# Kernel optimization log

Measured on AMD Instinct MI355X. Metric: run time of the kernel, lower is better.

## Reference

```python
import jax, jax.numpy as jnp
import numpy as np

D_MODEL = 1024


def setup_inputs() -> dict:
    key = jax.random.key(0)
    ks = jax.random.split(key, 7)
    x = jax.random.normal(ks[0], (4, 2048, D_MODEL), dtype=jnp.float32)
    scale = 1.0 / np.sqrt(D_MODEL)
    Wq = jax.random.normal(ks[1], (D_MODEL, D_MODEL), dtype=jnp.float32) * scale
    bq = jnp.zeros((D_MODEL,), dtype=jnp.float32)
    Wk = jax.random.normal(ks[2], (D_MODEL, D_MODEL), dtype=jnp.float32) * scale
    bk = jnp.zeros((D_MODEL,), dtype=jnp.float32)
    Wv = jax.random.normal(ks[3], (D_MODEL, D_MODEL), dtype=jnp.float32) * scale
    bv = jnp.zeros((D_MODEL,), dtype=jnp.float32)
    return {"x": x, "Wq": Wq, "bq": bq, "Wk": Wk, "bk": bk, "Wv": Wv, "bv": bv}


def reference(x, Wq, bq, Wk, bk, Wv, bv):
    # Linear layers: y = x @ W^T + b (torch nn.Linear convention)
    q = jnp.einsum("bsd,ed->bse", x, Wq) + bq
    k = jnp.einsum("bsd,ed->bse", x, Wk) + bk
    v = jnp.einsum("bsd,ed->bse", x, Wv) + bv
    d_k = q.shape[-1]
    inv_sqrt_dk = 1.0 / jnp.sqrt(jnp.float32(d_k))
    # [B, S, S] score matrix, softmax over keys, then AV
    score = jnp.einsum("bqd,bkd->bqk", q, k) * inv_sqrt_dk
    attn = jax.nn.softmax(score, axis=-1)
    out = jnp.einsum("bqk,bkd->bqd", attn, v)
    return out
```

## Files before the change

### kernel.cpp

```cpp
#include <hip/hip_runtime.h>
#include <hip/hip_bf16.h>


typedef __hip_bfloat16 bf16;
typedef __attribute__((ext_vector_type(8))) short bf16x8;
typedef __attribute__((ext_vector_type(4))) float f32x4;
typedef __attribute__((ext_vector_type(4))) short short4v;

__device__ __forceinline__ void gload16(const void* g, void* l) {
  __builtin_amdgcn_global_load_lds(
      (const __attribute__((address_space(1))) void*)g,
      (__attribute__((address_space(3))) void*)l, 16, 0, 0);
}

__global__ __launch_bounds__(256)
void cast_f32_to_bf16(const float* __restrict__ in, bf16* __restrict__ out) {
  long i = ((long)blockIdx.x * blockDim.x + threadIdx.x) * 4;
  float4 f = *(const float4*)(in + i);
  bf16 tmp[4];
  tmp[0] = __float2bfloat16(f.x);
  tmp[1] = __float2bfloat16(f.y);
  tmp[2] = __float2bfloat16(f.z);
  tmp[3] = __float2bfloat16(f.w);
  *(short4v*)(out + i) = *(short4v*)tmp;
}

template<int OMODE>
__global__ __launch_bounds__(256, 3)
void gemm_bt(const bf16* __restrict__ A, const bf16* __restrict__ Bt,
             const float* __restrict__ b0, const float* __restrict__ b1,
             const float* __restrict__ b2, void* __restrict__ Cout,
             int K, int lda, int ldb, int ldc, float scale,
             long sA, long sB, long sC)
{
  __shared__ __align__(16) bf16 As[128 * 64];
  __shared__ __align__(16) bf16 Bs[128 * 64];
  const int tid = threadIdx.x;
  const int z = blockIdx.z;
  const bf16* Ab = A + (long)z * sA;
  const bf16* Bb = Bt + (long)z * sB;
  const long bm = (long)blockIdx.x * 128;
  const long bn = (long)blockIdx.y * 128;
  const int wid = tid >> 6;
  const int lane = tid & 63;
  const int wr = (wid >> 1) * 64;
  const int wc = (wid & 1) * 64;
  const int l15 = lane & 15;
  const int kg = lane >> 4;

  f32x4 acc[4][4];
#pragma unroll
  for (int m = 0; m < 4; ++m)
#pragma unroll
    for (int n = 0; n < 4; ++n)
      acc[m][n] = (f32x4){0.f, 0.f, 0.f, 0.f};

  for (int k0 = 0; k0 < K; k0 += 64) {
#pragma unroll
    for (int i = 0; i < 4; ++i) {
      const int c = (i << 8) + tid;
      const int r = c >> 3;
      const int j = (c & 7) ^ (r & 7);
      const int ldsch = (i << 8) + (wid << 6);
      gload16(Ab + (long)(bm + r) * lda + k0 + (j << 3), (bf16*)As + ldsch * 8);
      gload16(Bb + (long)(bn + r) * ldb + k0 + (j << 3), (bf16*)Bs + ldsch * 8);
    }
    __syncthreads();
#pragma unroll
    for (int kk = 0; kk < 2; ++kk) {
      const int jp = ((kk << 2) + kg) ^ (l15 & 7);
      bf16x8 af[4], bfv[4];
#pragma unroll
      for (int m = 0; m < 4; ++m)
        af[m] = *(const bf16x8*)&As[(wr + (m << 4) + l15) * 64 + (jp << 3)];
#pragma unroll
      for (int n = 0; n < 4; ++n)
        bfv[n] = *(const bf16x8*)&Bs[(wc + (n << 4) + l15) * 64 + (jp << 3)];
#pragma unroll
      for (int m = 0; m < 4; ++m)
#pragma unroll
        for (int n = 0; n < 4; ++n)
          acc[m][n] = __builtin_amdgcn_mfma_f32_16x16x32_bf16(
              af[m], bfv[n], acc[m][n], 0, 0, 0);
    }
    __syncthreads();
  }

#pragma unroll
  for (int m = 0; m < 4; ++m) {
    const long row0 = bm + wr + (m << 4) + kg * 4;
#pragma unroll
    for (int n = 0; n < 4; ++n) {
      const long col = bn + wc + (n << 4) + l15;
      if constexpr (OMODE == 0) {
        float* C = (float*)Cout + z * sC;
#pragma unroll
        for (int r = 0; r < 4; ++r)
          C[(row0 + r) * ldc + col] = acc[m][n][r] * scale;
      } else {
        const float* bias = (z == 0) ? b0 : (z == 1) ? b1 : b2;
        const float bias_v = bias[col];
        if (z < 2) {
          bf16* C = (bf16*)Cout + (long)z * 8192 * 1024;
#pragma unroll
          for (int r = 0; r < 4; ++r)
            C[(row0 + r) * 1024 + col] = __float2bfloat16(acc[m][n][r] + bias_v);
        } else {
          bf16* C = (bf16*)Cout + 2L * 8192 * 1024;
          const long bb = row0 >> 11;
          const long s0 = row0 & 2047;
          bf16 tmp[4];
#pragma unroll
          for (int r = 0; r < 4; ++r)
            tmp[r] = __float2bfloat16(acc[m][n][r] + bias_v);
          *(short4v*)&C[(bb * 1024 + col) * 2048 + s0] = *(short4v*)tmp;
        }
      }
    }
  }
}

__global__ __launch_bounds__(256)
void softmax_inplace_bf16(float* __restrict__ S) {
  float* row = S + (size_t)blockIdx.x * 2048;
  const int tid = threadIdx.x;
  __shared__ float redA[4], redB[4];
  float v[8];
  float mx = -1e30f;
#pragma unroll
  for (int i = 0; i < 8; ++i) {
    v[i] = row[tid + (i << 8)];
    mx = fmaxf(mx, v[i]);
  }
#pragma unroll
  for (int o = 32; o; o >>= 1) mx = fmaxf(mx, __shfl_xor(mx, o));
  if ((tid & 63) == 0) redA[tid >> 6] = mx;
  __syncthreads();
  mx = fmaxf(fmaxf(redA[0], redA[1]), fmaxf(redA[2], redA[3]));
  float sum = 0.f;
#pragma unroll
  for (int i = 0; i < 8; ++i) {
    v[i] = __expf(v[i] - mx);
    sum += v[i];
  }
#pragma unroll
  for (int o = 32; o; o >>= 1) sum += __shfl_xor(sum, o);
  if ((tid & 63) == 0) redB[tid >> 6] = sum;
  __syncthreads();
  sum = redB[0] + redB[1] + redB[2] + redB[3];
  const float inv = 1.f / sum;
  bf16* po = (bf16*)row;
#pragma unroll
  for (int i = 0; i < 8; ++i)
    po[tid + (i << 8)] = __float2bfloat16(v[i] * inv);
}

extern "C" void kernel_launch(void* const* d_in, const int* in_sizes, int n_in,
                              void* d_out, int out_size, void* d_ws, size_t ws_size,
                              hipStream_t stream) {
  const float* x  = (const float*)d_in[0];
  const float* Wq = (const float*)d_in[1];
  const float* bq = (const float*)d_in[2];
  const float* Wk = (const float*)d_in[3];
  const float* bk = (const float*)d_in[4];
  const float* Wv = (const float*)d_in[5];
  const float* bv = (const float*)d_in[6];
  float* out = (float*)d_out;

  const int B = 4, S = 2048, D = 1024;
  const int M = B * S;

  bf16* xb  = (bf16*)d_ws;
  bf16* wqb = xb + (size_t)M * D;
  bf16* qb  = wqb + 3 * (size_t)D * D;
  bf16* kb  = qb + (size_t)M * D;
  bf16* vtb = kb + (size_t)M * D;
  float* sc = (float*)(vtb + (size_t)M * D);

  size_t avail = ws_size - ((size_t)((char*)sc - (char*)d_ws));
  int nb = (int)(avail / ((size_t)S * S * 4));
  if (nb > B) nb = B;
  if (nb < 1) nb = 1;

  cast_f32_to_bf16<<<dim3(M * D / 1024), 256, 0, stream>>>(x, xb);
  cast_f32_to_bf16<<<dim3(D * D / 1024), 256, 0, stream>>>(Wq, wqb);
  cast_f32_to_bf16<<<dim3(D * D / 1024), 256, 0, stream>>>(Wk, wqb + (size_t)D * D);
  cast_f32_to_bf16<<<dim3(D * D / 1024), 256, 0, stream>>>(Wv, wqb + 2 * (size_t)D * D);

  gemm_bt<3><<<dim3(M / 128, D / 128, 3), 256, 0, stream>>>(
      xb, wqb, bq, bk, bv, qb, D, D, D, D, 1.f, 0, (long)D * D, 0);

  const float iscale = 1.0f / 32.0f;
  for (int g = 0; g < B; g += nb) {
    const int gn = (g + nb <= B) ? nb : (B - g);
    gemm_bt<0><<<dim3(S / 128, S / 128, gn), 256, 0, stream>>>(
        qb + (size_t)g * S * D, kb + (size_t)g * S * D, nullptr, nullptr, nullptr,
        sc, D, D, D, S, iscale, (long)S * D, (long)S * D, (long)S * S);
    softmax_inplace_bf16<<<dim3(gn * S), 256, 0, stream>>>(sc);
    gemm_bt<0><<<dim3(S / 128, D / 128, gn), 256, 0, stream>>>(
        (const bf16*)sc, vtb + (size_t)g * D * S, nullptr, nullptr, nullptr,
        out + (size_t)g * S * D, S, 2 * S, S, D, 1.f,
        2L * S * S, (long)D * S, (long)S * D);
  }
}
```

Measured before the change: 178.7 us.

## Replace GEMMs with 8-wave double-buffered pipelined kernels and XCD-aware block remap

Replaces the single-buffered 128x128 GEMM with two 512-thread kernels: a 256x256 tile for QK^T and a 256x128 tile for the projection and AV GEMMs. Both double-buffer LDS and interleave global-to-LDS prefetch of the next K-slice with MFMA phases, using explicit vmcnt waits, sched barriers and s_setprio. Blocks are remapped so consecutive tiles land on the same XCD for L2 reuse. The larger tiles raise operand reuse and hide load latency, at the cost of higher LDS and register use per block, which lowers occupancy. The hand-counted waitcnt values add correctness risk.

```diff
diff --git a/kernel.cpp b/kernel.cpp
--- a/kernel.cpp
+++ b/kernel.cpp
@@ -7,11 +7,18 @@
 typedef __attribute__((ext_vector_type(4))) float f32x4;
 typedef __attribute__((ext_vector_type(4))) short short4v;
 
-__device__ __forceinline__ void gload16(const void* g, void* l) {
+__device__ __forceinline__ void gload16(const bf16* g, bf16* l) {
   __builtin_amdgcn_global_load_lds(
       (const __attribute__((address_space(1))) void*)g,
       (__attribute__((address_space(3))) void*)l, 16, 0, 0);
 }
+
+#define WAITV(N) asm volatile("s_waitcnt vmcnt(" #N ")" ::: "memory")
+#define LGKM0   asm volatile("s_waitcnt lgkmcnt(0)" ::: "memory")
+#define SCHED0  __builtin_amdgcn_sched_barrier(0)
+#define BAR     __builtin_amdgcn_s_barrier()
+#define PRIO1   __builtin_amdgcn_s_setprio(1)
+#define PRIO0   __builtin_amdgcn_s_setprio(0)
 
 __global__ __launch_bounds__(256)
 void cast_f32_to_bf16(const float* __restrict__ in, bf16* __restrict__ out) {
@@ -25,99 +32,302 @@
   *(short4v*)(out + i) = *(short4v*)tmp;
 }
 
+__device__ __forceinline__ void xcd_coords(int& bx, int& by, int& bz) {
+  const int gx = gridDim.x, gy = gridDim.y;
+  const int nwg = gx * gy * gridDim.z;
+  int n0 = blockIdx.x + gx * (blockIdx.y + gy * blockIdx.z);
+  int q = nwg >> 3, r = nwg & 7;
+  int xcd = n0 & 7, idx = n0 >> 3;
+  int n1 = (xcd < r ? xcd * (q + 1) : r * (q + 1) + (xcd - r) * q) + idx;
+  bz = n1 / (gx * gy);
+  int rem = n1 % (gx * gy);
+  by = rem / gx;
+  bx = rem % gx;
+}
+
+__global__ __launch_bounds__(512)
+void gemm8p_n256(const bf16* __restrict__ A, const bf16* __restrict__ Bt,
+                 float* __restrict__ C, int K, int lda, int ldb, int ldc,
+                 float scale, long sA, long sB, long sC)
+{
+  __shared__ __align__(16) bf16 As[2][256 * 64];
+  __shared__ __align__(16) bf16 Bs[2][256 * 64];
+  const int tid = threadIdx.x;
+  const int wid = tid >> 6, lane = tid & 63, l15 = lane & 15, kg = lane >> 4;
+  const int wr = wid >> 2, wc = wid & 3;
+  int bxi, byi, bz;
+  xcd_coords(bxi, byi, bz);
+  const long bm = (long)bxi * 256, bn = (long)byi * 256;
+  const bf16* Ab = A + (long)bz * sA;
+  const bf16* Bb = Bt + (long)bz * sB;
+
+  const bf16 *srcA0[2], *srcA1[2], *srcB0[2], *srcB1[2];
+  int ldsA0[2], ldsA1[2], ldsB0[2], ldsB1[2];
+#pragma unroll
+  for (int l = 0; l < 2; ++l) {
+    const int s = l * 512 + tid;
+    const int r0 = s >> 3;
+    {
+      int row = (r0 < 64) ? r0 : r0 + 64;
+      int j = (s & 7) ^ (row & 7);
+      srcA0[l] = Ab + (bm + row) * lda + (j << 3);
+      ldsA0[l] = (l ? 1024 : 0) + (wid << 6);
+    }
+    {
+      int row = (r0 < 64) ? r0 + 64 : r0 + 128;
+      int j = (s & 7) ^ (row & 7);
+      srcA1[l] = Ab + (bm + row) * lda + (j << 3);
+      ldsA1[l] = (l ? 1536 : 512) + (wid << 6);
+    }
+    {
+      int row = ((r0 >> 5) << 6) + (r0 & 31);
+      int j = (s & 7) ^ (row & 7);
+      srcB0[l] = Bb + (bn + row) * ldb + (j << 3);
+      int r0b = (l << 6) + (wid << 3);
+      ldsB0[l] = ((((r0b >> 5) << 6) + (r0b & 31)) << 3);
+    }
+    {
+      int row = ((r0 >> 5) << 6) + 32 + (r0 & 31);
+      int j = (s & 7) ^ (row & 7);
+      srcB1[l] = Bb + (bn + row) * ldb + (j << 3);
+      int r0b = (l << 6) + (wid << 3);
+      ldsB1[l] = ((((r0b >> 5) << 6) + 32 + (r0b & 31)) << 3);
+    }
+  }
+
+#define STG(SRC, LDS, NX, K0)                                         \
+  do { _Pragma("unroll") for (int l = 0; l < 2; ++l)                  \
+    gload16(SRC[l] + (K0), &((NX)[(LDS[l]) << 3])); } while (0)
+
+  bf16x8 af[2][4], b0f[2][2], b1f[2][2];
+  f32x4 acc[8][4];
+#pragma unroll
+  for (int m = 0; m < 8; ++m)
+#pragma unroll
+    for (int n = 0; n < 4; ++n) acc[m][n] = (f32x4){0.f, 0.f, 0.f, 0.f};
+
+#define READ_A(CUR, MH)                                               \
+  do { _Pragma("unroll") for (int kk = 0; kk < 2; ++kk)               \
+    _Pragma("unroll") for (int mi = 0; mi < 4; ++mi) {                \
+      int row_l = wr * 128 + ((MH) * 4 + mi) * 16 + l15;              \
+      int js = ((kk << 2) + kg) ^ (row_l & 7);                        \
+      af[kk][mi] = *(const bf16x8*)&(CUR)[(row_l << 6) + (js << 3)];  \
+    } } while (0)
+#define READ_B(CUR, NH, DST)                                          \
+  do { _Pragma("unroll") for (int kk = 0; kk < 2; ++kk)               \
+    _Pragma("unroll") for (int ni = 0; ni < 2; ++ni) {                \
+      int row_l = wc * 64 + ((NH) * 2 + ni) * 16 + l15;               \
+      int js = ((kk << 2) + kg) ^ (row_l & 7);                        \
+      DST[kk][ni] = *(const bf16x8*)&(CUR)[(row_l << 6) + (js << 3)]; \
+    } } while (0)
+#define MFMA16(MH, NH, BF)                                            \
+  do { _Pragma("unroll") for (int kk = 0; kk < 2; ++kk)               \
+    _Pragma("unroll") for (int mi = 0; mi < 4; ++mi)                  \
+    _Pragma("unroll") for (int ni = 0; ni < 2; ++ni)                  \
+      acc[(MH)*4+mi][(NH)*2+ni] = __builtin_amdgcn_mfma_f32_16x16x32_bf16( \
+          af[kk][mi], BF[kk][ni], acc[(MH)*4+mi][(NH)*2+ni], 0, 0, 0);\
+  } while (0)
+
+  const int T = K >> 6;
+  STG(srcA0, ldsA0, As[0], 0);
+  STG(srcB0, ldsB0, Bs[0], 0);
+  STG(srcB1, ldsB1, Bs[0], 0);
+  STG(srcA1, ldsA1, As[0], 0);
+  WAITV(4);
+  BAR;
+
+  for (int t = 0; t < T; ++t) {
+    bf16* Ac = As[t & 1];
+    bf16* Bc = Bs[t & 1];
+    bf16* An = As[(t & 1) ^ 1];
+    bf16* Bn = Bs[(t & 1) ^ 1];
+    const int kn = (t + 1) << 6;
+    const bool pre = (t + 1) < T;
+    READ_A(Ac, 0);
+    READ_B(Bc, 0, b0f);
+    if (pre) { STG(srcA0, ldsA0, An, kn); STG(srcB0, ldsB0, Bn, kn); }
+    if (pre) WAITV(6); else WAITV(2);
+    BAR; LGKM0; SCHED0; PRIO1;
+    MFMA16(0, 0, b0f);
+    PRIO0; SCHED0; BAR;
+    READ_B(Bc, 1, b1f);
+    if (pre) STG(srcB1, ldsB1, Bn, kn);
+    if (pre) WAITV(6); else WAITV(0);
+    BAR; LGKM0; SCHED0; PRIO1;
+    MFMA16(0, 1, b1f);
+    PRIO0; SCHED0; BAR;
+    READ_A(Ac, 1);
+    if (pre) STG(srcA1, ldsA1, An, kn);
+    BAR; LGKM0; SCHED0; PRIO1;
+    MFMA16(1, 0, b0f);
+    PRIO0; SCHED0; BAR;
+    if (pre) WAITV(4);
+    BAR; PRIO1;
+    MFMA16(1, 1, b1f);
+    PRIO0; SCHED0; BAR;
+  }
+
+  float* Cz = C + (long)bz * sC;
+#pragma unroll
+  for (int m = 0; m < 8; ++m) {
+    const long row0 = bm + wr * 128 + m * 16 + (kg << 2);
+#pragma unroll
+    for (int n = 0; n < 4; ++n) {
+      const long col = bn + wc * 64 + n * 16 + l15;
+#pragma unroll
+      for (int rr = 0; rr < 4; ++rr)
+        Cz[(row0 + rr) * ldc + col] = acc[m][n][rr] * scale;
+    }
+  }
+#undef READ_A
+#undef READ_B
+#undef MFMA16
+#undef STG
+}
+
 template<int OMODE>
-__global__ __launch_bounds__(256, 3)
-void gemm_bt(const bf16* __restrict__ A, const bf16* __restrict__ Bt,
-             const float* __restrict__ b0, const float* __restrict__ b1,
-             const float* __restrict__ b2, void* __restrict__ Cout,
-             int K, int lda, int ldb, int ldc, float scale,
-             long sA, long sB, long sC)
+__global__ __launch_bounds__(512)
+void gemm8p_n128(const bf16* __restrict__ A, const bf16* __restrict__ Bt,
+                 const float* __restrict__ b0, const float* __restrict__ b1,
+                 const float* __restrict__ b2, void* __restrict__ Cout,
+                 int K, int lda, int ldb, int ldc, float scale,
+                 long sA, long sB, long sC)
 {
-  __shared__ __align__(16) bf16 As[128 * 64];
-  __shared__ __align__(16) bf16 Bs[128 * 64];
+  __shared__ __align__(16) bf16 As[2][256 * 64];
+  __shared__ __align__(16) bf16 Bs[2][128 * 64];
   const int tid = threadIdx.x;
-  const int z = blockIdx.z;
-  const bf16* Ab = A + (long)z * sA;
-  const bf16* Bb = Bt + (long)z * sB;
-  const long bm = (long)blockIdx.x * 128;
-  const long bn = (long)blockIdx.y * 128;
-  const int wid = tid >> 6;
-  const int lane = tid & 63;
-  const int wr = (wid >> 1) * 64;
-  const int wc = (wid & 1) * 64;
-  const int l15 = lane & 15;
-  const int kg = lane >> 4;
-
-  f32x4 acc[4][4];
-#pragma unroll
-  for (int m = 0; m < 4; ++m)
-#pragma unroll
-    for (int n = 0; n < 4; ++n)
-      acc[m][n] = (f32x4){0.f, 0.f, 0.f, 0.f};
-
-  for (int k0 = 0; k0 < K; k0 += 64) {
-#pragma unroll
-    for (int i = 0; i < 4; ++i) {
-      const int c = (i << 8) + tid;
-      const int r = c >> 3;
-      const int j = (c & 7) ^ (r & 7);
-      const int ldsch = (i << 8) + (wid << 6);
-      gload16(Ab + (long)(bm + r) * lda + k0 + (j << 3), (bf16*)As + ldsch * 8);
-      gload16(Bb + (long)(bn + r) * ldb + k0 + (j << 3), (bf16*)Bs + ldsch * 8);
-    }
-    __syncthreads();
-#pragma unroll
-    for (int kk = 0; kk < 2; ++kk) {
-      const int jp = ((kk << 2) + kg) ^ (l15 & 7);
-      bf16x8 af[4], bfv[4];
-#pragma unroll
-      for (int m = 0; m < 4; ++m)
-        af[m] = *(const bf16x8*)&As[(wr + (m << 4) + l15) * 64 + (jp << 3)];
-#pragma unroll
-      for (int n = 0; n < 4; ++n)
-        bfv[n] = *(const bf16x8*)&Bs[(wc + (n << 4) + l15) * 64 + (jp << 3)];
-#pragma unroll
-      for (int m = 0; m < 4; ++m)
-#pragma unroll
-        for (int n = 0; n < 4; ++n)
-          acc[m][n] = __builtin_amdgcn_mfma_f32_16x16x32_bf16(
-              af[m], bfv[n], acc[m][n], 0, 0, 0);
-    }
-    __syncthreads();
-  }
-
-#pragma unroll
-  for (int m = 0; m < 4; ++m) {
-    const long row0 = bm + wr + (m << 4) + kg * 4;
-#pragma unroll
-    for (int n = 0; n < 4; ++n) {
-      const long col = bn + wc + (n << 4) + l15;
+  const int wid = tid >> 6, lane = tid & 63, l15 = lane & 15, kg = lane >> 4;
+  const int wr = wid >> 2, wc = wid & 3;
+  int bxi, byi, bz;
+  xcd_coords(bxi, byi, bz);
+  const long bm = (long)bxi * 256, bn = (long)byi * 128;
+  const bf16* Ab = A + (long)bz * sA;
+  const bf16* Bb = Bt + (long)bz * sB;
+
+  const bf16 *srcA0[2], *srcA1[2], *srcBw[2];
+  int ldsA0[2], ldsA1[2], ldsBw[2];
+#pragma unroll
+  for (int l = 0; l < 2; ++l) {
+    const int s = l * 512 + tid;
+    const int r0 = s >> 3;
+    {
+      int row = (r0 < 64) ? r0 : r0 + 64;
+      int j = (s & 7) ^ (row & 7);
+      srcA0[l] = Ab + (bm + row) * lda + (j << 3);
+      ldsA0[l] = (l ? 1024 : 0) + (wid << 6);
+    }
+    {
+      int row = (r0 < 64) ? r0 + 64 : r0 + 128;
+      int j = (s & 7) ^ (row & 7);
+      srcA1[l] = Ab + (bm + row) * lda + (j << 3);
+      ldsA1[l] = (l ? 1536 : 512) + (wid << 6);
+    }
+    {
+      int row = r0;
+      int j = (s & 7) ^ (row & 7);
+      srcBw[l] = Bb + (bn + row) * ldb + (j << 3);
+      ldsBw[l] = l * 512 + (wid << 6);
+    }
+  }
+
+#define STG(SRC, LDS, NX, K0)                                         \
+  do { _Pragma("unroll") for (int l = 0; l < 2; ++l)                  \
+    gload16(SRC[l] + (K0), &((NX)[(LDS[l]) << 3])); } while (0)
+
+  bf16x8 af[2][4], bf_[2][2];
+  f32x4 acc[8][2];
+#pragma unroll
+  for (int m = 0; m < 8; ++m)
+#pragma unroll
+    for (int n = 0; n < 2; ++n) acc[m][n] = (f32x4){0.f, 0.f, 0.f, 0.f};
+
+#define READ_A(CUR, MH)                                               \
+  do { _Pragma("unroll") for (int kk = 0; kk < 2; ++kk)               \
+    _Pragma("unroll") for (int mi = 0; mi < 4; ++mi) {                \
+      int row_l = wr * 128 + ((MH) * 4 + mi) * 16 + l15;              \
+      int js = ((kk << 2) + kg) ^ (row_l & 7);                        \
+      af[kk][mi] = *(const bf16x8*)&(CUR)[(row_l << 6) + (js << 3)];  \
+    } } while (0)
+#define READ_B(CUR)                                                   \
+  do { _Pragma("unroll") for (int kk = 0; kk < 2; ++kk)               \
+    _Pragma("unroll") for (int ni = 0; ni < 2; ++ni) {                \
+      int row_l = wc * 32 + ni * 16 + l15;                            \
+      int js = ((kk << 2) + kg) ^ (row_l & 7);                        \
+      bf_[kk][ni] = *(const bf16x8*)&(CUR)[(row_l << 6) + (js << 3)]; \
+    } } while (0)
+#define MFMA16(MH)                                                    \
+  do { _Pragma("unroll") for (int kk = 0; kk < 2; ++kk)               \
+    _Pragma("unroll") for (int mi = 0; mi < 4; ++mi)                  \
+    _Pragma("unroll") for (int ni = 0; ni < 2; ++ni)                  \
+      acc[(MH)*4+mi][ni] = __builtin_amdgcn_mfma_f32_16x16x32_bf16(   \
+          af[kk][mi], bf_[kk][ni], acc[(MH)*4+mi][ni], 0, 0, 0);      \
+  } while (0)
+
+  const int T = K >> 6;
+  STG(srcA0, ldsA0, As[0], 0);
+  STG(srcBw, ldsBw, Bs[0], 0);
+  STG(srcA1, ldsA1, As[0], 0);
+  WAITV(2);
+  BAR;
+
+  for (int t = 0; t < T; ++t) {
+    bf16* Ac = As[t & 1];
+    bf16* Bc = Bs[t & 1];
+    bf16* An = As[(t & 1) ^ 1];
+    bf16* Bn = Bs[(t & 1) ^ 1];
+    const int kn = (t + 1) << 6;
+    const bool pre = (t + 1) < T;
+    READ_A(Ac, 0);
+    READ_B(Bc);
+    if (pre) { STG(srcA0, ldsA0, An, kn); STG(srcBw, ldsBw, Bn, kn); }
+    if (pre) WAITV(4); else WAITV(0);
+    BAR; LGKM0; SCHED0; PRIO1;
+    MFMA16(0);
+    PRIO0; SCHED0; BAR;
+    READ_A(Ac, 1);
+    if (pre) STG(srcA1, ldsA1, An, kn);
+    if (pre) WAITV(2);
+    BAR; LGKM0; SCHED0; PRIO1;
+    MFMA16(1);
+    PRIO0; SCHED0; BAR;
+  }
+
+#pragma unroll
+  for (int m = 0; m < 8; ++m) {
+    const long row0 = bm + wr * 128 + m * 16 + (kg << 2);
+#pragma unroll
+    for (int n = 0; n < 2; ++n) {
+      const long col = bn + wc * 32 + n * 16 + l15;
       if constexpr (OMODE == 0) {
-        float* C = (float*)Cout + z * sC;
-#pragma unroll
-        for (int r = 0; r < 4; ++r)
-          C[(row0 + r) * ldc + col] = acc[m][n][r] * scale;
+        float* C = (float*)Cout + (long)bz * sC;
+#pragma unroll
+        for (int rr = 0; rr < 4; ++rr)
+          C[(row0 + rr) * ldc + col] = acc[m][n][rr] * scale;
       } else {
-        const float* bias = (z == 0) ? b0 : (z == 1) ? b1 : b2;
+        const float* bias = (bz == 0) ? b0 : (bz == 1) ? b1 : b2;
         const float bias_v = bias[col];
-        if (z < 2) {
-          bf16* C = (bf16*)Cout + (long)z * 8192 * 1024;
-#pragma unroll
-          for (int r = 0; r < 4; ++r)
-            C[(row0 + r) * 1024 + col] = __float2bfloat16(acc[m][n][r] + bias_v);
+        if (bz < 2) {
+          bf16* C = (bf16*)Cout + (long)bz * 8192 * 1024;
+#pragma unroll
+          for (int rr = 0; rr < 4; ++rr)
+            C[(row0 + rr) * 1024 + col] = __float2bfloat16(acc[m][n][rr] + bias_v);
         } else {
           bf16* C = (bf16*)Cout + 2L * 8192 * 1024;
           const long bb = row0 >> 11;
           const long s0 = row0 & 2047;
           bf16 tmp[4];
 #pragma unroll
-          for (int r = 0; r < 4; ++r)
-            tmp[r] = __float2bfloat16(acc[m][n][r] + bias_v);
+          for (int rr = 0; rr < 4; ++rr)
+            tmp[rr] = __float2bfloat16(acc[m][n][rr] + bias_v);
           *(short4v*)&C[(bb * 1024 + col) * 2048 + s0] = *(short4v*)tmp;
         }
       }
     }
   }
+#undef READ_A
+#undef READ_B
+#undef MFMA16
+#undef STG
 }
 
 __global__ __launch_bounds__(256)
@@ -187,17 +397,17 @@
   cast_f32_to_bf16<<<dim3(D * D / 1024), 256, 0, stream>>>(Wk, wqb + (size_t)D * D);
   cast_f32_to_bf16<<<dim3(D * D / 1024), 256, 0, stream>>>(Wv, wqb + 2 * (size_t)D * D);
 
-  gemm_bt<3><<<dim3(M / 128, D / 128, 3), 256, 0, stream>>>(
+  gemm8p_n128<3><<<dim3(M / 256, D / 128, 3), 512, 0, stream>>>(
       xb, wqb, bq, bk, bv, qb, D, D, D, D, 1.f, 0, (long)D * D, 0);
 
   const float iscale = 1.0f / 32.0f;
   for (int g = 0; g < B; g += nb) {
     const int gn = (g + nb <= B) ? nb : (B - g);
-    gemm_bt<0><<<dim3(S / 128, S / 128, gn), 256, 0, stream>>>(
-        qb + (size_t)g * S * D, kb + (size_t)g * S * D, nullptr, nullptr, nullptr,
-        sc, D, D, D, S, iscale, (long)S * D, (long)S * D, (long)S * S);
+    gemm8p_n256<<<dim3(S / 256, S / 256, gn), 512, 0, stream>>>(
+        qb + (size_t)g * S * D, kb + (size_t)g * S * D, sc,
+        D, D, D, S, iscale, (long)S * D, (long)S * D, (long)S * S);
     softmax_inplace_bf16<<<dim3(gn * S), 256, 0, stream>>>(sc);
-    gemm_bt<0><<<dim3(S / 128, D / 128, gn), 256, 0, stream>>>(
+    gemm8p_n128<0><<<dim3(S / 256, D / 128, gn), 512, 0, stream>>>(
         (const bf16*)sc, vtb + (size_t)g * D * S, nullptr, nullptr, nullptr,
         out + (size_t)g * S * D, S, 2 * S, S, D, 1.f,
         2L * S * S, (long)D * S, (long)S * D);
```

New measurement: 197.1 us. +10.3%, slower.

## Replace GEMMs with 256-tile double-buffered pipelined MFMA kernels

Applied to the files above, without the earlier changes.

Replaces the 128x128 single-buffered GEMM with a 256x256 tile kernel (512 threads, 8 waves) that double-buffers LDS, interleaves async global-to-LDS loads with MFMA phases, and uses explicit waitcnt, sched barriers and setprio. The QKV projection becomes a single launch that treats the three weight matrices as one 3072-wide N dimension. A separate 256x128 pipelined kernel handles the PV product. The aim is to hide memory latency and raise data reuse per tile, at the cost of larger LDS use (128KB), lower occupancy and more register pressure.

```diff
diff --git a/kernel.cpp b/kernel.cpp
--- a/kernel.cpp
+++ b/kernel.cpp
@@ -7,11 +7,18 @@
 typedef __attribute__((ext_vector_type(4))) float f32x4;
 typedef __attribute__((ext_vector_type(4))) short short4v;
 
-__device__ __forceinline__ void gload16(const void* g, void* l) {
+__device__ __forceinline__ void gload16(const bf16* g, bf16* l) {
   __builtin_amdgcn_global_load_lds(
       (const __attribute__((address_space(1))) void*)g,
       (__attribute__((address_space(3))) void*)l, 16, 0, 0);
 }
+
+#define WAITV(N) asm volatile("s_waitcnt vmcnt(" #N ")" ::: "memory")
+#define LGKM0    asm volatile("s_waitcnt lgkmcnt(0)" ::: "memory")
+#define SCHED0   __builtin_amdgcn_sched_barrier(0)
+#define BAR      __builtin_amdgcn_s_barrier()
+#define PRIO1    __builtin_amdgcn_s_setprio(1)
+#define PRIO0    __builtin_amdgcn_s_setprio(0)
 
 __global__ __launch_bounds__(256)
 void cast_f32_to_bf16(const float* __restrict__ in, bf16* __restrict__ out) {
@@ -26,98 +33,240 @@
 }
 
 template<int OMODE>
-__global__ __launch_bounds__(256, 3)
-void gemm_bt(const bf16* __restrict__ A, const bf16* __restrict__ Bt,
-             const float* __restrict__ b0, const float* __restrict__ b1,
-             const float* __restrict__ b2, void* __restrict__ Cout,
-             int K, int lda, int ldb, int ldc, float scale,
-             long sA, long sB, long sC)
+__global__ __launch_bounds__(512)
+void gemm256(const bf16* __restrict__ A, const bf16* __restrict__ Bt,
+             int K, int lda, int ldb,
+             float* __restrict__ Cf, int ldc, float scale,
+             long sA, long sB, long sC,
+             bf16* __restrict__ qout, bf16* __restrict__ kout,
+             bf16* __restrict__ vtout,
+             const float* __restrict__ bqp, const float* __restrict__ bkp,
+             const float* __restrict__ bvp)
 {
-  __shared__ __align__(16) bf16 As[128 * 64];
-  __shared__ __align__(16) bf16 Bs[128 * 64];
+  __shared__ __align__(16) bf16 As[2][256 * 64];
+  __shared__ __align__(16) bf16 Bs[2][256 * 64];
   const int tid = threadIdx.x;
-  const int z = blockIdx.z;
-  const bf16* Ab = A + (long)z * sA;
-  const bf16* Bb = Bt + (long)z * sB;
-  const long bm = (long)blockIdx.x * 128;
-  const long bn = (long)blockIdx.y * 128;
-  const int wid = tid >> 6;
-  const int lane = tid & 63;
-  const int wr = (wid >> 1) * 64;
-  const int wc = (wid & 1) * 64;
-  const int l15 = lane & 15;
-  const int kg = lane >> 4;
-
-  f32x4 acc[4][4];
-#pragma unroll
-  for (int m = 0; m < 4; ++m)
-#pragma unroll
-    for (int n = 0; n < 4; ++n)
-      acc[m][n] = (f32x4){0.f, 0.f, 0.f, 0.f};
-
-  for (int k0 = 0; k0 < K; k0 += 64) {
-#pragma unroll
-    for (int i = 0; i < 4; ++i) {
-      const int c = (i << 8) + tid;
-      const int r = c >> 3;
-      const int j = (c & 7) ^ (r & 7);
-      const int ldsch = (i << 8) + (wid << 6);
-      gload16(Ab + (long)(bm + r) * lda + k0 + (j << 3), (bf16*)As + ldsch * 8);
-      gload16(Bb + (long)(bn + r) * ldb + k0 + (j << 3), (bf16*)Bs + ldsch * 8);
-    }
-    __syncthreads();
-#pragma unroll
-    for (int kk = 0; kk < 2; ++kk) {
-      const int jp = ((kk << 2) + kg) ^ (l15 & 7);
-      bf16x8 af[4], bfv[4];
-#pragma unroll
-      for (int m = 0; m < 4; ++m)
-        af[m] = *(const bf16x8*)&As[(wr + (m << 4) + l15) * 64 + (jp << 3)];
-#pragma unroll
-      for (int n = 0; n < 4; ++n)
-        bfv[n] = *(const bf16x8*)&Bs[(wc + (n << 4) + l15) * 64 + (jp << 3)];
-#pragma unroll
-      for (int m = 0; m < 4; ++m)
-#pragma unroll
-        for (int n = 0; n < 4; ++n)
-          acc[m][n] = __builtin_amdgcn_mfma_f32_16x16x32_bf16(
-              af[m], bfv[n], acc[m][n], 0, 0, 0);
-    }
-    __syncthreads();
-  }
-
-#pragma unroll
-  for (int m = 0; m < 4; ++m) {
-    const long row0 = bm + wr + (m << 4) + kg * 4;
+  const int wid = tid >> 6, lane = tid & 63, l15 = lane & 15, kg = lane >> 4;
+  const int wr = wid >> 2, wc = wid & 3;
+  const int bz = blockIdx.z;
+  const long bm = (long)blockIdx.x * 256, bn = (long)blockIdx.y * 256;
+  const bf16* Ab = A + (long)bz * sA;
+  const bf16* Bb = Bt + (long)bz * sB;
+
+  const bf16* gsrc[8];
+  int ldst[8];
+#pragma unroll
+  for (int g = 0; g < 8; ++g) {
+    const bool isB = g >= 4;
+    const int half = (g >> 1) & 1;
+    const int l = g & 1;
+    const int c = half * 1024 + l * 512 + tid;
+    const int r = c >> 3;
+    const int j = (c & 7) ^ (r & 7);
+    gsrc[g] = isB ? (Bb + (bn + r) * (long)ldb + (j << 3))
+                  : (Ab + (bm + r) * (long)lda + (j << 3));
+    ldst[g] = c << 3;
+  }
+#define STG2(G, BUF, K0) do {                      \
+    gload16(gsrc[G] + (K0), &(BUF)[ldst[G]]);      \
+    gload16(gsrc[(G)+1] + (K0), &(BUF)[ldst[(G)+1]]); } while (0)
+
+  bf16x8 af[2][4], b0f[2][2], b1f[2][2];
+  f32x4 acc[8][4];
+#pragma unroll
+  for (int m = 0; m < 8; ++m)
+#pragma unroll
+    for (int n = 0; n < 4; ++n) acc[m][n] = (f32x4){0.f, 0.f, 0.f, 0.f};
+
+#define READ_A(P, MH)                                                   \
+  do { _Pragma("unroll") for (int kk = 0; kk < 2; ++kk)                 \
+    _Pragma("unroll") for (int mi = 0; mi < 4; ++mi) {                  \
+      int row_l = wr * 128 + ((MH) * 4 + mi) * 16 + l15;                \
+      int js = ((kk << 2) + kg) ^ (row_l & 7);                          \
+      af[kk][mi] = *(const bf16x8*)&(P)[(row_l << 6) + (js << 3)];      \
+    } } while (0)
+#define READ_B(P, NH, DST)                                              \
+  do { _Pragma("unroll") for (int kk = 0; kk < 2; ++kk)                 \
+    _Pragma("unroll") for (int ni = 0; ni < 2; ++ni) {                  \
+      int row_l = wc * 64 + ((NH) * 2 + ni) * 16 + l15;                 \
+      int js = ((kk << 2) + kg) ^ (row_l & 7);                          \
+      DST[kk][ni] = *(const bf16x8*)&(P)[(row_l << 6) + (js << 3)];     \
+    } } while (0)
+#define MFMA16(MH, NH, BF)                                              \
+  do { _Pragma("unroll") for (int kk = 0; kk < 2; ++kk)                 \
+    _Pragma("unroll") for (int mi = 0; mi < 4; ++mi)                    \
+    _Pragma("unroll") for (int ni = 0; ni < 2; ++ni)                    \
+      acc[(MH)*4+mi][(NH)*2+ni] = __builtin_amdgcn_mfma_f32_16x16x32_bf16( \
+          af[kk][mi], BF[kk][ni], acc[(MH)*4+mi][(NH)*2+ni], 0, 0, 0);  \
+  } while (0)
+
+  const int T = K >> 6;
+  STG2(0, As[0], 0); STG2(4, Bs[0], 0); STG2(2, As[0], 0); STG2(6, Bs[0], 0);
+
+  for (int t = 0; t < T; t += 2) {
+    const int k1 = (t + 1) << 6, k2 = (t + 2) << 6;
+    const bool pre = (t + 2) < T;
+    STG2(0, As[1], k1); STG2(4, Bs[1], k1);
+    WAITV(4);
+    BAR;
+    READ_A(As[0], 0); READ_B(Bs[0], 0, b0f);
+    LGKM0; SCHED0; PRIO1; MFMA16(0, 0, b0f); PRIO0; BAR;
+    READ_B(Bs[0], 1, b1f);
+    STG2(2, As[1], k1); STG2(6, Bs[1], k1);
+    BAR; LGKM0; SCHED0; PRIO1; MFMA16(0, 1, b1f); PRIO0; BAR;
+    READ_A(As[0], 1);
+    BAR; LGKM0; SCHED0; PRIO1; MFMA16(1, 0, b0f); PRIO0; BAR;
+    PRIO1; MFMA16(1, 1, b1f); PRIO0; BAR;
+    if (pre) { STG2(0, As[0], k2); STG2(4, Bs[0], k2); WAITV(4); }
+    else WAITV(0);
+    BAR;
+    READ_A(As[1], 0); READ_B(Bs[1], 0, b0f);
+    LGKM0; SCHED0; PRIO1; MFMA16(0, 0, b0f); PRIO0; BAR;
+    READ_B(Bs[1], 1, b1f);
+    if (pre) { STG2(2, As[0], k2); STG2(6, Bs[0], k2); }
+    BAR; LGKM0; SCHED0; PRIO1; MFMA16(0, 1, b1f); PRIO0; BAR;
+    READ_A(As[1], 1);
+    BAR; LGKM0; SCHED0; PRIO1; MFMA16(1, 0, b0f); PRIO0; BAR;
+    PRIO1; MFMA16(1, 1, b1f); PRIO0; BAR;
+  }
+
+#pragma unroll
+  for (int m = 0; m < 8; ++m) {
+    const long row0 = bm + wr * 128 + m * 16 + (kg << 2);
 #pragma unroll
     for (int n = 0; n < 4; ++n) {
-      const long col = bn + wc + (n << 4) + l15;
+      const long col = bn + wc * 64 + n * 16 + l15;
       if constexpr (OMODE == 0) {
-        float* C = (float*)Cout + z * sC;
-#pragma unroll
-        for (int r = 0; r < 4; ++r)
-          C[(row0 + r) * ldc + col] = acc[m][n][r] * scale;
+        float* C = Cf + (long)bz * sC;
+#pragma unroll
+        for (int rr = 0; rr < 4; ++rr)
+          C[(row0 + rr) * ldc + col] = acc[m][n][rr] * scale;
       } else {
-        const float* bias = (z == 0) ? b0 : (z == 1) ? b1 : b2;
-        const float bias_v = bias[col];
-        if (z < 2) {
-          bf16* C = (bf16*)Cout + (long)z * 8192 * 1024;
-#pragma unroll
-          for (int r = 0; r < 4; ++r)
-            C[(row0 + r) * 1024 + col] = __float2bfloat16(acc[m][n][r] + bias_v);
+        const int mat = (int)(col >> 10);
+        const long c1 = col & 1023;
+        if (mat < 2) {
+          const float bias_v = (mat ? bkp : bqp)[c1];
+          bf16* C = mat ? kout : qout;
+#pragma unroll
+          for (int rr = 0; rr < 4; ++rr)
+            C[(row0 + rr) * 1024 + c1] = __float2bfloat16(acc[m][n][rr] + bias_v);
         } else {
-          bf16* C = (bf16*)Cout + 2L * 8192 * 1024;
+          const float bias_v = bvp[c1];
           const long bb = row0 >> 11;
           const long s0 = row0 & 2047;
           bf16 tmp[4];
 #pragma unroll
-          for (int r = 0; r < 4; ++r)
-            tmp[r] = __float2bfloat16(acc[m][n][r] + bias_v);
-          *(short4v*)&C[(bb * 1024 + col) * 2048 + s0] = *(short4v*)tmp;
+          for (int rr = 0; rr < 4; ++rr)
+            tmp[rr] = __float2bfloat16(acc[m][n][rr] + bias_v);
+          *(short4v*)&vtout[(bb * 1024 + c1) * 2048 + s0] = *(short4v*)tmp;
         }
       }
     }
   }
+#undef READ_A
+#undef READ_B
+#undef MFMA16
+#undef STG2
+}
+
+__global__ __launch_bounds__(512)
+void gemmPV(const bf16* __restrict__ A, const bf16* __restrict__ Bt,
+            float* __restrict__ C, int K, int lda, int ldb, int ldc,
+            long sA, long sB, long sC)
+{
+  __shared__ __align__(16) bf16 As[2][256 * 64];
+  __shared__ __align__(16) bf16 Bs[2][128 * 64];
+  const int tid = threadIdx.x;
+  const int wid = tid >> 6, lane = tid & 63, l15 = lane & 15, kg = lane >> 4;
+  const int wr = wid >> 2, wc = wid & 3;
+  const int bz = blockIdx.z;
+  const long bm = (long)blockIdx.x * 256, bn = (long)blockIdx.y * 128;
+  const bf16* Ab = A + (long)bz * sA;
+  const bf16* Bb = Bt + (long)bz * sB;
+
+  const bf16* gsrc[6];
+  int ldst[6];
+#pragma unroll
+  for (int g = 0; g < 6; ++g) {
+    const bool isB = g >= 4;
+    const int half = isB ? 0 : (g >> 1);
+    const int l = g & 1;
+    const int c = half * 1024 + l * 512 + tid;
+    const int r = c >> 3;
+    const int j = (c & 7) ^ (r & 7);
+    gsrc[g] = isB ? (Bb + (bn + r) * (long)ldb + (j << 3))
+                  : (Ab + (bm + r) * (long)lda + (j << 3));
+    ldst[g] = c << 3;
+  }
+#define STG2(G, BUF, K0) do {                      \
+    gload16(gsrc[G] + (K0), &(BUF)[ldst[G]]);      \
+    gload16(gsrc[(G)+1] + (K0), &(BUF)[ldst[(G)+1]]); } while (0)
+
+  bf16x8 af[2][4], bf_[2][2];
+  f32x4 acc[8][2];
+#pragma unroll
+  for (int m = 0; m < 8; ++m)
+#pragma unroll
+    for (int n = 0; n < 2; ++n) acc[m][n] = (f32x4){0.f, 0.f, 0.f, 0.f};
+
+#define READ_A(P, MH)                                                   \
+  do { _Pragma("unroll") for (int kk = 0; kk < 2; ++kk)                 \
+    _Pragma("unroll") for (int mi = 0; mi < 4; ++mi) {                  \
+      int row_l = wr * 128 + ((MH) * 4 + mi) * 16 + l15;                \
+      int js = ((kk << 2) + kg) ^ (row_l & 7);                          \
+      af[kk][mi] = *(const bf16x8*)&(P)[(row_l << 6) + (js << 3)];      \
+    } } while (0)
+#define READ_B(P)                                                       \
+  do { _Pragma("unroll") for (int kk = 0; kk < 2; ++kk)                 \
+    _Pragma("unroll") for (int ni = 0; ni < 2; ++ni) {                  \
+      int row_l = wc * 32 + ni * 16 + l15;                              \
+      int js = ((kk << 2) + kg) ^ (row_l & 7);                          \
+      bf_[kk][ni] = *(const bf16x8*)&(P)[(row_l << 6) + (js << 3)];     \
+    } } while (0)
+#define MFMA16(MH)                                                      \
+  do { _Pragma("unroll") for (int kk = 0; kk < 2; ++kk)                 \
+    _Pragma("unroll") for (int mi = 0; mi < 4; ++mi)                    \
+    _Pragma("unroll") for (int ni = 0; ni < 2; ++ni)                    \
+      acc[(MH)*4+mi][ni] = __builtin_amdgcn_mfma_f32_16x16x32_bf16(     \
+          af[kk][mi], bf_[kk][ni], acc[(MH)*4+mi][ni], 0, 0, 0);        \
+  } while (0)
+
+  const int T = K >> 6;
+  STG2(0, As[0], 0); STG2(4, Bs[0], 0); STG2(2, As[0], 0);
+
+  for (int t = 0; t < T; ++t) {
+    bf16* Ac = As[t & 1];
+    bf16* Bc = Bs[t & 1];
+    bf16* An = As[(t & 1) ^ 1];
+    bf16* Bn = Bs[(t & 1) ^ 1];
+    const int k1 = (t + 1) << 6;
+    const bool pre = (t + 1) < T;
+    if (pre) { STG2(0, An, k1); STG2(4, Bn, k1); WAITV(4); }
+    else WAITV(0);
+    BAR;
+    READ_A(Ac, 0); READ_B(Bc);
+    LGKM0; SCHED0; PRIO1; MFMA16(0); PRIO0; BAR;
+    READ_A(Ac, 1);
+    if (pre) STG2(2, An, k1);
+    BAR; LGKM0; SCHED0; PRIO1; MFMA16(1); PRIO0; BAR;
+  }
+
+#pragma unroll
+  for (int m = 0; m < 8; ++m) {
+    const long row0 = bm + wr * 128 + m * 16 + (kg << 2);
+#pragma unroll
+    for (int n = 0; n < 2; ++n) {
+      const long col = bn + wc * 32 + n * 16 + l15;
+      float* Cz = C + (long)bz * sC;
+#pragma unroll
+      for (int rr = 0; rr < 4; ++rr)
+        Cz[(row0 + rr) * ldc + col] = acc[m][n][rr];
+    }
+  }
+#undef READ_A
+#undef READ_B
+#undef MFMA16
+#undef STG2
 }
 
 __global__ __launch_bounds__(256)
@@ -187,19 +336,21 @@
   cast_f32_to_bf16<<<dim3(D * D / 1024), 256, 0, stream>>>(Wk, wqb + (size_t)D * D);
   cast_f32_to_bf16<<<dim3(D * D / 1024), 256, 0, stream>>>(Wv, wqb + 2 * (size_t)D * D);
 
-  gemm_bt<3><<<dim3(M / 128, D / 128, 3), 256, 0, stream>>>(
-      xb, wqb, bq, bk, bv, qb, D, D, D, D, 1.f, 0, (long)D * D, 0);
+  gemm256<1><<<dim3(M / 256, 3 * D / 256, 1), 512, 0, stream>>>(
+      xb, wqb, D, D, D, nullptr, 0, 1.f, 0, 0, 0,
+      qb, kb, vtb, bq, bk, bv);
 
   const float iscale = 1.0f / 32.0f;
   for (int g = 0; g < B; g += nb) {
     const int gn = (g + nb <= B) ? nb : (B - g);
-    gemm_bt<0><<<dim3(S / 128, S / 128, gn), 256, 0, stream>>>(
-        qb + (size_t)g * S * D, kb + (size_t)g * S * D, nullptr, nullptr, nullptr,
-        sc, D, D, D, S, iscale, (long)S * D, (long)S * D, (long)S * S);
+    gemm256<0><<<dim3(S / 256, S / 256, gn), 512, 0, stream>>>(
+        qb + (size_t)g * S * D, kb + (size_t)g * S * D, D, D, D,
+        sc, S, iscale, (long)S * D, (long)S * D, (long)S * S,
+        nullptr, nullptr, nullptr, nullptr, nullptr, nullptr);
     softmax_inplace_bf16<<<dim3(gn * S), 256, 0, stream>>>(sc);
-    gemm_bt<0><<<dim3(S / 128, D / 128, gn), 256, 0, stream>>>(
-        (const bf16*)sc, vtb + (size_t)g * D * S, nullptr, nullptr, nullptr,
-        out + (size_t)g * S * D, S, 2 * S, S, D, 1.f,
+    gemmPV<<<dim3(S / 256, D / 128, gn), 512, 0, stream>>>(
+        (const bf16*)sc, vtb + (size_t)g * D * S,
+        out + (size_t)g * S * D, S, 2 * S, S, D,
         2L * S * S, (long)D * S, (long)S * D);
   }
 }
```

New measurement: 214.9 us. 20.3% more time.

## Switch GEMMs to 32x32 MFMA and store scores as bf16 end-to-end

Applied to the files above, without the earlier changes.

Replaces the 16x16x32 MFMA tiling with 32x32x16 bf16 MFMA (2x2 per warp), which cuts LDS fragment loads per MFMA. The QK^T GEMM now writes scaled scores directly as bf16 instead of fp32, and softmax reads and writes bf16 with 16-byte vector accesses. This halves score-matrix traffic and lets more batches fit in the workspace at once. The trade-off is that scores are rounded to bf16 before softmax, which loses some precision.

```diff
diff --git a/kernel.cpp b/kernel.cpp
--- a/kernel.cpp
+++ b/kernel.cpp
@@ -4,10 +4,10 @@
 
 typedef __hip_bfloat16 bf16;
 typedef __attribute__((ext_vector_type(8))) short bf16x8;
-typedef __attribute__((ext_vector_type(4))) float f32x4;
+typedef __attribute__((ext_vector_type(16))) float f32x16;
 typedef __attribute__((ext_vector_type(4))) short short4v;
 
-__device__ __forceinline__ void gload16(const void* g, void* l) {
+__device__ __forceinline__ void gload16(const bf16* g, bf16* l) {
   __builtin_amdgcn_global_load_lds(
       (const __attribute__((address_space(1))) void*)g,
       (__attribute__((address_space(3))) void*)l, 16, 0, 0);
@@ -45,15 +45,16 @@
   const int lane = tid & 63;
   const int wr = (wid >> 1) * 64;
   const int wc = (wid & 1) * 64;
-  const int l15 = lane & 15;
-  const int kg = lane >> 4;
-
-  f32x4 acc[4][4];
-#pragma unroll
-  for (int m = 0; m < 4; ++m)
-#pragma unroll
-    for (int n = 0; n < 4; ++n)
-      acc[m][n] = (f32x4){0.f, 0.f, 0.f, 0.f};
+  const int fr = lane & 31;
+  const int kh = lane >> 5;
+
+  f32x16 acc[2][2];
+#pragma unroll
+  for (int m = 0; m < 2; ++m)
+#pragma unroll
+    for (int n = 0; n < 2; ++n)
+      acc[m][n] = (f32x16){0.f,0.f,0.f,0.f,0.f,0.f,0.f,0.f,
+                           0.f,0.f,0.f,0.f,0.f,0.f,0.f,0.f};
 
   for (int k0 = 0; k0 < K; k0 += 64) {
 #pragma unroll
@@ -62,58 +63,73 @@
       const int r = c >> 3;
       const int j = (c & 7) ^ (r & 7);
       const int ldsch = (i << 8) + (wid << 6);
-      gload16(Ab + (long)(bm + r) * lda + k0 + (j << 3), (bf16*)As + ldsch * 8);
-      gload16(Bb + (long)(bn + r) * ldb + k0 + (j << 3), (bf16*)Bs + ldsch * 8);
+      gload16(Ab + (long)(bm + r) * lda + k0 + (j << 3), As + ldsch * 8);
+      gload16(Bb + (long)(bn + r) * ldb + k0 + (j << 3), Bs + ldsch * 8);
     }
     __syncthreads();
 #pragma unroll
-    for (int kk = 0; kk < 2; ++kk) {
-      const int jp = ((kk << 2) + kg) ^ (l15 & 7);
-      bf16x8 af[4], bfv[4];
-#pragma unroll
-      for (int m = 0; m < 4; ++m)
-        af[m] = *(const bf16x8*)&As[(wr + (m << 4) + l15) * 64 + (jp << 3)];
-#pragma unroll
-      for (int n = 0; n < 4; ++n)
-        bfv[n] = *(const bf16x8*)&Bs[(wc + (n << 4) + l15) * 64 + (jp << 3)];
-#pragma unroll
-      for (int m = 0; m < 4; ++m)
-#pragma unroll
-        for (int n = 0; n < 4; ++n)
-          acc[m][n] = __builtin_amdgcn_mfma_f32_16x16x32_bf16(
+    for (int ks = 0; ks < 4; ++ks) {
+      bf16x8 af[2], bfv[2];
+#pragma unroll
+      for (int m = 0; m < 2; ++m) {
+        const int row_l = wr + (m << 5) + fr;
+        const int js = ((ks << 1) + kh) ^ (row_l & 7);
+        af[m] = *(const bf16x8*)&As[(row_l << 6) + (js << 3)];
+      }
+#pragma unroll
+      for (int n = 0; n < 2; ++n) {
+        const int row_l = wc + (n << 5) + fr;
+        const int js = ((ks << 1) + kh) ^ (row_l & 7);
+        bfv[n] = *(const bf16x8*)&Bs[(row_l << 6) + (js << 3)];
+      }
+#pragma unroll
+      for (int m = 0; m < 2; ++m)
+#pragma unroll
+        for (int n = 0; n < 2; ++n)
+          acc[m][n] = __builtin_amdgcn_mfma_f32_32x32x16_bf16(
               af[m], bfv[n], acc[m][n], 0, 0, 0);
     }
     __syncthreads();
   }
 
 #pragma unroll
-  for (int m = 0; m < 4; ++m) {
-    const long row0 = bm + wr + (m << 4) + kg * 4;
-#pragma unroll
-    for (int n = 0; n < 4; ++n) {
-      const long col = bn + wc + (n << 4) + l15;
-      if constexpr (OMODE == 0) {
-        float* C = (float*)Cout + z * sC;
-#pragma unroll
-        for (int r = 0; r < 4; ++r)
-          C[(row0 + r) * ldc + col] = acc[m][n][r] * scale;
-      } else {
-        const float* bias = (z == 0) ? b0 : (z == 1) ? b1 : b2;
-        const float bias_v = bias[col];
-        if (z < 2) {
-          bf16* C = (bf16*)Cout + (long)z * 8192 * 1024;
-#pragma unroll
-          for (int r = 0; r < 4; ++r)
-            C[(row0 + r) * 1024 + col] = __float2bfloat16(acc[m][n][r] + bias_v);
+  for (int m = 0; m < 2; ++m) {
+#pragma unroll
+    for (int n = 0; n < 2; ++n) {
+      const long col = bn + wc + (n << 5) + fr;
+#pragma unroll
+      for (int g = 0; g < 4; ++g) {
+        const long row0 = bm + wr + (m << 5) + (g << 3) + (kh << 2);
+        if constexpr (OMODE == 0) {
+          float* C = (float*)Cout + (long)z * sC;
+#pragma unroll
+          for (int rr = 0; rr < 4; ++rr)
+            C[(row0 + rr) * ldc + col] = acc[m][n][(g << 2) + rr] * scale;
+        } else if constexpr (OMODE == 1) {
+          bf16* C = (bf16*)Cout + (long)z * sC;
+#pragma unroll
+          for (int rr = 0; rr < 4; ++rr)
+            C[(row0 + rr) * ldc + col] =
+                __float2bfloat16(acc[m][n][(g << 2) + rr] * scale);
         } else {
-          bf16* C = (bf16*)Cout + 2L * 8192 * 1024;
-          const long bb = row0 >> 11;
-          const long s0 = row0 & 2047;
-          bf16 tmp[4];
-#pragma unroll
-          for (int r = 0; r < 4; ++r)
-            tmp[r] = __float2bfloat16(acc[m][n][r] + bias_v);
-          *(short4v*)&C[(bb * 1024 + col) * 2048 + s0] = *(short4v*)tmp;
+          const float* bias = (z == 0) ? b0 : (z == 1) ? b1 : b2;
+          const float bias_v = bias[col];
+          if (z < 2) {
+            bf16* C = (bf16*)Cout + (long)z * 8192 * 1024;
+#pragma unroll
+            for (int rr = 0; rr < 4; ++rr)
+              C[(row0 + rr) * 1024 + col] =
+                  __float2bfloat16(acc[m][n][(g << 2) + rr] + bias_v);
+          } else {
+            bf16* C = (bf16*)Cout + 2L * 8192 * 1024;
+            const long bb = row0 >> 11;
+            const long s0 = row0 & 2047;
+            bf16 tmp[4];
+#pragma unroll
+            for (int rr = 0; rr < 4; ++rr)
+              tmp[rr] = __float2bfloat16(acc[m][n][(g << 2) + rr] + bias_v);
+            *(short4v*)&C[(bb * 1024 + col) * 2048 + s0] = *(short4v*)tmp;
+          }
         }
       }
     }
@@ -121,15 +137,16 @@
 }
 
 __global__ __launch_bounds__(256)
-void softmax_inplace_bf16(float* __restrict__ S) {
-  float* row = S + (size_t)blockIdx.x * 2048;
+void softmax_bf16(bf16* __restrict__ S) {
+  bf16* row = S + (size_t)blockIdx.x * 2048;
   const int tid = threadIdx.x;
   __shared__ float redA[4], redB[4];
+  bf16x8 in = *(const bf16x8*)(row + (tid << 3));
   float v[8];
   float mx = -1e30f;
 #pragma unroll
   for (int i = 0; i < 8; ++i) {
-    v[i] = row[tid + (i << 8)];
+    v[i] = __bfloat162float(((const bf16*)&in)[i]);
     mx = fmaxf(mx, v[i]);
   }
 #pragma unroll
@@ -149,10 +166,10 @@
   __syncthreads();
   sum = redB[0] + redB[1] + redB[2] + redB[3];
   const float inv = 1.f / sum;
-  bf16* po = (bf16*)row;
-#pragma unroll
-  for (int i = 0; i < 8; ++i)
-    po[tid + (i << 8)] = __float2bfloat16(v[i] * inv);
+  bf16 tmp[8];
+#pragma unroll
+  for (int i = 0; i < 8; ++i) tmp[i] = __float2bfloat16(v[i] * inv);
+  *(bf16x8*)(row + (tid << 3)) = *(bf16x8*)tmp;
 }
 
 extern "C" void kernel_launch(void* const* d_in, const int* in_sizes, int n_in,
@@ -175,10 +192,10 @@
   bf16* qb  = wqb + 3 * (size_t)D * D;
   bf16* kb  = qb + (size_t)M * D;
   bf16* vtb = kb + (size_t)M * D;
-  float* sc = (float*)(vtb + (size_t)M * D);
+  bf16* sc  = vtb + (size_t)M * D;
 
   size_t avail = ws_size - ((size_t)((char*)sc - (char*)d_ws));
-  int nb = (int)(avail / ((size_t)S * S * 4));
+  int nb = (int)(avail / ((size_t)S * S * 2));
   if (nb > B) nb = B;
   if (nb < 1) nb = 1;
 
@@ -193,13 +210,13 @@
   const float iscale = 1.0f / 32.0f;
   for (int g = 0; g < B; g += nb) {
     const int gn = (g + nb <= B) ? nb : (B - g);
-    gemm_bt<0><<<dim3(S / 128, S / 128, gn), 256, 0, stream>>>(
+    gemm_bt<1><<<dim3(S / 128, S / 128, gn), 256, 0, stream>>>(
         qb + (size_t)g * S * D, kb + (size_t)g * S * D, nullptr, nullptr, nullptr,
         sc, D, D, D, S, iscale, (long)S * D, (long)S * D, (long)S * S);
-    softmax_inplace_bf16<<<dim3(gn * S), 256, 0, stream>>>(sc);
+    softmax_bf16<<<dim3(gn * S), 256, 0, stream>>>(sc);
     gemm_bt<0><<<dim3(S / 128, D / 128, gn), 256, 0, stream>>>(
-        (const bf16*)sc, vtb + (size_t)g * D * S, nullptr, nullptr, nullptr,
-        out + (size_t)g * S * D, S, 2 * S, S, D, 1.f,
-        2L * S * S, (long)D * S, (long)S * D);
-  }
-}
+        sc, vtb + (size_t)g * D * S, nullptr, nullptr, nullptr,
+        out + (size_t)g * S * D, S, S, S, D, 1.f,
+        (long)S * S, (long)D * S, (long)S * D);
+  }
+}
```

Result: slower. 190.8 us (+6.8%).
